# Kernel optimization log

Measured on AMD Instinct MI355X. Metric: run time of the kernel, lower is better.

Reference implementation:

```python
import jax, jax.numpy as jnp
import numpy as np

N_NODES = 50000
N_EDGES = 800000
IN_CH, HID_CH, OUT_CH = 128, 128, 64


def setup_inputs() -> dict:
    key = jax.random.key(0)
    k1, k2, k3, k4 = jax.random.split(key, 4)
    x = jax.random.normal(k1, (N_NODES, IN_CH), dtype=jnp.float32)
    edge_index = jax.random.randint(k2, (2, N_EDGES), 0, N_NODES, dtype=jnp.int64)
    W1 = jax.random.normal(k3, (IN_CH, HID_CH), dtype=jnp.float32) * (1.0 / np.sqrt(IN_CH))
    b1 = jnp.zeros((HID_CH,), dtype=jnp.float32)
    W2 = jax.random.normal(k4, (HID_CH, OUT_CH), dtype=jnp.float32) * (1.0 / np.sqrt(HID_CH))
    b2 = jnp.zeros((OUT_CH,), dtype=jnp.float32)
    return {"x": x, "edge_index": edge_index, "W1": W1, "b1": b1, "W2": W2, "b2": b2}


def _gcn_conv(x, src, dst, norm, W, b, n_nodes):
    # x' = D^-1/2 (A+I) D^-1/2 (x W) + b
    h = x @ W                                        # [N, C_out]
    msg = norm[:, None] * h[src]                     # gather + scale, [E', C_out]
    agg = jax.ops.segment_sum(msg, dst, num_segments=n_nodes)
    return agg + b


def reference(x, edge_index, W1, b1, W2, b2):
    n = x.shape[0]
    # add self loops
    loops = jnp.arange(n, dtype=edge_index.dtype)
    src = jnp.concatenate([edge_index[0], loops])
    dst = jnp.concatenate([edge_index[1], loops])
    # symmetric degree normalization computed on target index
    deg = jax.ops.segment_sum(jnp.ones_like(dst, dtype=x.dtype), dst, num_segments=n)
    dinv = jnp.where(deg > 0, jax.lax.rsqrt(deg), 0.0)
    norm = dinv[src] * dinv[dst]                     # [E']

    h = jax.nn.relu(_gcn_conv(x, src, dst, norm, W1, b1, n))
    logits = _gcn_conv(h, src, dst, norm, W2, b2, n)
    return jax.nn.softmax(logits, axis=1)
```

## Files before the change

### kernel.cpp

```cpp
#include <hip/hip_runtime.h>
#include <hip/hip_fp16.h>


#define SLOT 64
#define NB   49
#define CAP  18432
#define EPB  4096

typedef _Float16 h4 __attribute__((ext_vector_type(4)));
typedef _Float16 h8 __attribute__((ext_vector_type(8)));
typedef float f4 __attribute__((ext_vector_type(4)));

__global__ __launch_bounds__(256) void k_prep(const int* __restrict__ ei,
                                              int* __restrict__ bcur,
                                              unsigned int* __restrict__ bkt,
                                              const float* __restrict__ W1,
                                              const float* __restrict__ W2,
                                              _Float16* __restrict__ W1p,
                                              _Float16* __restrict__ W2p,
                                              int e, int pb) {
    __shared__ int sSrc[EPB];
    __shared__ int sDst[EPB];
    __shared__ int sCnt[64];
    if (blockIdx.x < pb) {
        int b0 = blockIdx.x * EPB;
        int cnt = min(EPB, e - b0);
        for (int i = threadIdx.x; i < cnt; i += 256) {
            sSrc[i] = ei[b0 + i];
            sDst[i] = ei[e + b0 + i];
        }
        if (threadIdx.x < 64) sCnt[threadIdx.x] = 0;
        __syncthreads();
        for (int i = threadIdx.x; i < cnt; i += 256)
            atomicAdd(&sCnt[sDst[i] >> 10], 1);
        __syncthreads();
        if (threadIdx.x < 64) {
            int c = sCnt[threadIdx.x];
            int gbase = (c > 0 && threadIdx.x < NB) ? atomicAdd(&bcur[threadIdx.x], c) : 0;
            sCnt[threadIdx.x] = gbase;
        }
        __syncthreads();
        for (int i = threadIdx.x; i < cnt; i += 256) {
            int d = sDst[i];
            int b = d >> 10;
            int pos = atomicAdd(&sCnt[b], 1);
            if (pos < CAP)
                bkt[(size_t)b * CAP + pos] =
                    ((unsigned int)(d & 1023) << 16) | (unsigned int)sSrc[i];
        }
    } else {
        int i = (blockIdx.x - pb) * 256 + threadIdx.x;
        float w; int k, c; _Float16* dst;
        if (i < 16384)      { k = i >> 7, c = i & 127; w = W1[i]; dst = W1p; }
        else if (i < 24576) { int t = i - 16384; k = t >> 6; c = t & 63; w = W2[t]; dst = W2p; }
        else return;
        _Float16 hi = (_Float16)w;
        _Float16 lo = (_Float16)(w - (float)hi);
        int kc = k >> 4, kk = k & 15;
        int l = (kk >> 2) * 16 + (c & 15);
        int j = kk & 3;
        int ct = c >> 4;
        size_t base = ((size_t)(ct * 8 + kc) * 64 + l) * 8 + j;
        dst[base] = hi;
        dst[base + 4] = lo;
    }
}

__global__ __launch_bounds__(256) void k_main1(
    const int* __restrict__ bcur, const unsigned int* __restrict__ bkt,
    unsigned short* __restrict__ csr, int* __restrict__ deg,
    float* __restrict__ dinv,
    const float* __restrict__ X, const _Float16* __restrict__ Wp,
    __half* __restrict__ H, int n, int bb)
{
    __shared__ unsigned short rows[256 * SLOT];
    __shared__ int cur[256];
    if (blockIdx.x < bb) {
        int r = blockIdx.x;
        int b = r >> 2;
        int q = r & 3;
        cur[threadIdx.x] = 0;
        __syncthreads();
        int cnt = min(bcur[b], CAP);
        const unsigned int* bp = bkt + (size_t)b * CAP;
        for (int i = threadIdx.x; i < cnt; i += 256) {
            unsigned int p = bp[i];
            int dl = (int)(p >> 16);
            if ((dl >> 8) == q) {
                int node = dl & 255;
                int pos = atomicAdd(&cur[node], 1);
                if (pos < SLOT) rows[node * SLOT + pos] = (unsigned short)(p & 0xffff);
            }
        }
        __syncthreads();
        int base = r * 256;
        uint4* dst4 = (uint4*)(csr + (size_t)base * SLOT);
        const uint4* src4 = (const uint4*)rows;
        for (int i = threadIdx.x; i < 256 * SLOT / 8; i += 256) dst4[i] = src4[i];
        int node = base + threadIdx.x;
        if (node < n) {
            int c = cur[threadIdx.x];
            deg[node] = c;
            dinv[node] = rsqrtf((float)(c + 1));
        }
    } else {
        int blk = blockIdx.x - bb;
        int w = threadIdx.x >> 6, lane = threadIdx.x & 63;
        int r0 = blk * 64 + w * 16;
        int xr = r0 + (lane & 15);
        int xrc = min(xr, n - 1);
        const float* xp = X + (size_t)xrc * 128 + ((lane >> 4) * 4);

        f4 acc[8];
#pragma unroll
        for (int ct = 0; ct < 8; ++ct) acc[ct] = (f4){0.f, 0.f, 0.f, 0.f};

#pragma unroll
        for (int kc = 0; kc < 8; ++kc) {
            float4 xv = *(const float4*)(xp + kc * 16);
            h4 xh, xl;
            xh[0] = (_Float16)xv.x; xh[1] = (_Float16)xv.y;
            xh[2] = (_Float16)xv.z; xh[3] = (_Float16)xv.w;
            xl[0] = (_Float16)(xv.x - (float)xh[0]);
            xl[1] = (_Float16)(xv.y - (float)xh[1]);
            xl[2] = (_Float16)(xv.z - (float)xh[2]);
            xl[3] = (_Float16)(xv.w - (float)xh[3]);
#pragma unroll
            for (int ct = 0; ct < 8; ++ct) {
                h8 wb = ((const h8*)Wp)[(ct * 8 + kc) * 64 + lane];
                h4 wh = {wb[0], wb[1], wb[2], wb[3]};
                h4 wl = {wb[4], wb[5], wb[6], wb[7]};
                acc[ct] = __builtin_amdgcn_mfma_f32_16x16x16f16(wh, xh, acc[ct], 0, 0, 0);
                acc[ct] = __builtin_amdgcn_mfma_f32_16x16x16f16(wl, xh, acc[ct], 0, 0, 0);
                acc[ct] = __builtin_amdgcn_mfma_f32_16x16x16f16(wh, xl, acc[ct], 0, 0, 0);
            }
        }
        if (xr < n) {
            __half* hp = H + (size_t)xr * 128 + (lane >> 4) * 4;
#pragma unroll
            for (int ct = 0; ct < 8; ++ct) {
                h4 o = {(_Float16)acc[ct][0], (_Float16)acc[ct][1],
                        (_Float16)acc[ct][2], (_Float16)acc[ct][3]};
                *(h4*)(hp + ct * 16) = o;
            }
        }
    }
}

__global__ __launch_bounds__(256) void k_agg1(
    const int* __restrict__ deg, const unsigned short* __restrict__ csr,
    const float* __restrict__ dinv, const __half* __restrict__ H,
    const float* __restrict__ b1, __half* __restrict__ H1, int n)
{
    int node = blockIdx.x * 4 + (threadIdx.x >> 6);
    if (node >= n) return;
    int lane = threadIdx.x & 63;
    int g = lane >> 4, sub = lane & 15;
    float dd = dinv[node];

    float acc[8];
#pragma unroll
    for (int i = 0; i < 8; ++i) acc[i] = 0.f;

    int beg = node * SLOT;
    int cnt = min(deg[node], SLOT);
    {
        int m = cnt;
        int   s_l = (lane < m) ? (int)csr[beg + lane] : 0;
        float w_l = (lane < m) ? dinv[s_l] * dd : 0.f;
        int iters = (m + 3) >> 2;
#pragma unroll 4
        for (int t = 0; t < iters; ++t) {
            int j = 4 * t + g;
            int   s = __shfl(s_l, j);
            float w = __shfl(w_l, j);
            float4 raw = ((const float4*)(H + (size_t)s * 128))[sub];
            const __half2* h2 = (const __half2*)&raw;
#pragma unroll
            for (int q = 0; q < 4; ++q) {
                float2 v = __half22float2(h2[q]);
                acc[2 * q]     = fmaf(w, v.x, acc[2 * q]);
                acc[2 * q + 1] = fmaf(w, v.y, acc[2 * q + 1]);
            }
        }
    }
#pragma unroll
    for (int i = 0; i < 8; ++i) {
        acc[i] += __shfl_xor(acc[i], 16);
        acc[i] += __shfl_xor(acc[i], 32);
    }
    float4 sraw = ((const float4*)(H + (size_t)node * 128))[sub];
    const __half2* sh2 = (const __half2*)&sraw;
    float sl = dd * dd;
    float4 bb0 = ((const float4*)(b1 + sub * 8))[0];
    float4 bb1 = ((const float4*)(b1 + sub * 8))[1];
    float out[8];
#pragma unroll
    for (int q = 0; q < 4; ++q) {
        float2 v = __half22float2(sh2[q]);
        out[2 * q]     = fmaf(sl, v.x, acc[2 * q]);
        out[2 * q + 1] = fmaf(sl, v.y, acc[2 * q + 1]);
    }
    out[0] += bb0.x; out[1] += bb0.y; out[2] += bb0.z; out[3] += bb0.w;
    out[4] += bb1.x; out[5] += bb1.y; out[6] += bb1.z; out[7] += bb1.w;
    if (g == 0) {
        h8 o;
#pragma unroll
        for (int i = 0; i < 8; ++i) o[i] = (_Float16)fmaxf(out[i], 0.f);
        *(h8*)(H1 + (size_t)node * 128 + sub * 8) = o;
    }
}

__global__ __launch_bounds__(256) void k_gemm2(
    const __half* __restrict__ Xh, const _Float16* __restrict__ Wp,
    __half* __restrict__ H2, int n)
{
    int w = threadIdx.x >> 6, lane = threadIdx.x & 63;
    int r0 = blockIdx.x * 64 + w * 16;
    int xr = r0 + (lane & 15);
    int xrc = min(xr, n - 1);
    const _Float16* xp = (const _Float16*)Xh + (size_t)xrc * 128 + ((lane >> 4) * 4);

    f4 acc[4];
#pragma unroll
    for (int ct = 0; ct < 4; ++ct) acc[ct] = (f4){0.f, 0.f, 0.f, 0.f};

#pragma unroll
    for (int kc = 0; kc < 8; ++kc) {
        h4 xh = *(const h4*)(xp + kc * 16);
#pragma unroll
        for (int ct = 0; ct < 4; ++ct) {
            h8 wb = ((const h8*)Wp)[(ct * 8 + kc) * 64 + lane];
            h4 wh = {wb[0], wb[1], wb[2], wb[3]};
            h4 wl = {wb[4], wb[5], wb[6], wb[7]};
            acc[ct] = __builtin_amdgcn_mfma_f32_16x16x16f16(wh, xh, acc[ct], 0, 0, 0);
            acc[ct] = __builtin_amdgcn_mfma_f32_16x16x16f16(wl, xh, acc[ct], 0, 0, 0);
        }
    }
    if (xr < n) {
        __half* hp = H2 + (size_t)xr * 64 + (lane >> 4) * 4;
#pragma unroll
        for (int ct = 0; ct < 4; ++ct) {
            h4 o = {(_Float16)acc[ct][0], (_Float16)acc[ct][1],
                    (_Float16)acc[ct][2], (_Float16)acc[ct][3]};
            *(h4*)(hp + ct * 16) = o;
        }
    }
}

__global__ __launch_bounds__(256) void k_agg2(
    const int* __restrict__ deg, const unsigned short* __restrict__ csr,
    const float* __restrict__ dinv, const __half* __restrict__ H2,
    const float* __restrict__ b2, float* __restrict__ OUT, int n)
{
    int node = blockIdx.x * 4 + (threadIdx.x >> 6);
    if (node >= n) return;
    int lane = threadIdx.x & 63;
    int g = lane >> 3, sub = lane & 7;
    float dd = dinv[node];

    float acc[8];
#pragma unroll
    for (int i = 0; i < 8; ++i) acc[i] = 0.f;

    int beg = node * SLOT;
    int cnt = min(deg[node], SLOT);
    {
        int m = cnt;
        int   s_l = (lane < m) ? (int)csr[beg + lane] : 0;
        float w_l = (lane < m) ? dinv[s_l] * dd : 0.f;
        int iters = (m + 7) >> 3;
#pragma unroll 4
        for (int t = 0; t < iters; ++t) {
            int j = 8 * t + g;
            int   s = __shfl(s_l, j);
            float w = __shfl(w_l, j);
            float4 raw = ((const float4*)(H2 + (size_t)s * 64))[sub];
            const __half2* h2 = (const __half2*)&raw;
#pragma unroll
            for (int q = 0; q < 4; ++q) {
                float2 v = __half22float2(h2[q]);
                acc[2 * q]     = fmaf(w, v.x, acc[2 * q]);
                acc[2 * q + 1] = fmaf(w, v.y, acc[2 * q + 1]);
            }
        }
    }
#pragma unroll
    for (int i = 0; i < 8; ++i) {
        acc[i] += __shfl_xor(acc[i], 8);
        acc[i] += __shfl_xor(acc[i], 16);
        acc[i] += __shfl_xor(acc[i], 32);
    }
    float4 sraw = ((const float4*)(H2 + (size_t)node * 64))[sub];
    const __half2* sh2 = (const __half2*)&sraw;
    float sl = dd * dd;
    float4 bb0 = ((const float4*)(b2 + sub * 8))[0];
    float4 bb1 = ((const float4*)(b2 + sub * 8))[1];
    float out[8];
#pragma unroll
    for (int q = 0; q < 4; ++q) {
        float2 v = __half22float2(sh2[q]);
        out[2 * q]     = fmaf(sl, v.x, acc[2 * q]);
        out[2 * q + 1] = fmaf(sl, v.y, acc[2 * q + 1]);
    }
    out[0] += bb0.x; out[1] += bb0.y; out[2] += bb0.z; out[3] += bb0.w;
    out[4] += bb1.x; out[5] += bb1.y; out[6] += bb1.z; out[7] += bb1.w;
    float mx = out[0];
#pragma unroll
    for (int i = 1; i < 8; ++i) mx = fmaxf(mx, out[i]);
    mx = fmaxf(mx, __shfl_xor(mx, 1));
    mx = fmaxf(mx, __shfl_xor(mx, 2));
    mx = fmaxf(mx, __shfl_xor(mx, 4));
    float sm = 0.f;
#pragma unroll
    for (int i = 0; i < 8; ++i) { out[i] = expf(out[i] - mx); sm += out[i]; }
    sm += __shfl_xor(sm, 1);
    sm += __shfl_xor(sm, 2);
    sm += __shfl_xor(sm, 4);
    float inv = 1.f / sm;
#pragma unroll
    for (int i = 0; i < 8; ++i) out[i] *= inv;
    float* op = OUT + (size_t)node * 64 + sub * 8;
    if (g == 0) *(float4*)op       = make_float4(out[0], out[1], out[2], out[3]);
    if (g == 1) *(float4*)(op + 4) = make_float4(out[4], out[5], out[6], out[7]);
}

extern "C" void kernel_launch(void* const* d_in, const int* in_sizes, int n_in,
                              void* d_out, int out_size, void* d_ws, size_t ws_size,
                              hipStream_t stream) {
    const float* X  = (const float*)d_in[0];
    const int*   EI = (const int*)d_in[1];
    const float* W1 = (const float*)d_in[2];
    const float* B1 = (const float*)d_in[3];
    const float* W2 = (const float*)d_in[4];
    const float* B2 = (const float*)d_in[5];
    float* OUT = (float*)d_out;

    const int n = in_sizes[0] / 128;
    const int e = in_sizes[1] / 2;

    const int np = (n + 255) & ~255;
    int*            bcur = (int*)d_ws;
    int*            deg  = bcur + 64;
    float*          dinv = (float*)(deg + np);
    unsigned int*   bkt  = (unsigned int*)(dinv + np);
    unsigned short* csr  = (unsigned short*)(bkt + (size_t)NB * CAP);
    _Float16*       W1p  = (_Float16*)(csr + (size_t)np * SLOT);
    _Float16*       W2p  = W1p + 32768;
    __half*         H16  = (__half*)(W2p + 16384);
    __half*         H1   = (__half*)(H16 + (size_t)np * 128);
    __half*         H2   = H1 + (size_t)np * 128;

    const int pb = (e + EPB - 1) / EPB;
    const int bb = np / 256;
    const int gb = (n + 63) / 64;

    (void)hipMemsetAsync(bcur, 0, 64 * sizeof(int), stream);
    k_prep<<<pb + 96, 256, 0, stream>>>(EI, bcur, bkt, W1, W2, W1p, W2p, e, pb);
    k_main1<<<bb + gb, 256, 0, stream>>>(bcur, bkt, csr, deg, dinv,
                                         X, W1p, H16, n, bb);
    k_agg1<<<(n + 3) / 4, 256, 0, stream>>>(deg, csr, dinv, H16, B1, H1, n);
    k_gemm2<<<gb, 256, 0, stream>>>(H1, W2p, H2, n);
    k_agg2<<<(n + 3) / 4, 256, 0, stream>>>(deg, csr, dinv, H2, B2, OUT, n);
}
```

Measured before the change: 194.1 us.

## Fuse second-layer GEMM into first aggregation kernel using wave shuffles

Replaces the separate MFMA GEMM for layer 2 with per-node shuffle-broadcast FMAs inside the layer-1 aggregation kernel, writing H2 directly. This removes the H1 intermediate's global write and reread and one kernel launch, and drops W2 prepacking. In exchange, every wave does 128 shuffles and 128 W2 loads per node on scalar FMA units instead of tensor cores, which may make the aggregation kernel compute- or load-bound.

```diff
diff --git a/kernel.cpp b/kernel.cpp
--- a/kernel.cpp
+++ b/kernel.cpp
@@ -15,14 +15,12 @@
                                               int* __restrict__ bcur,
                                               unsigned int* __restrict__ bkt,
                                               const float* __restrict__ W1,
-                                              const float* __restrict__ W2,
                                               _Float16* __restrict__ W1p,
-                                              _Float16* __restrict__ W2p,
                                               int e, int pb) {
     __shared__ int sSrc[EPB];
     __shared__ int sDst[EPB];
     __shared__ int sCnt[64];
-    if (blockIdx.x < pb) {
+    if ((int)blockIdx.x < pb) {
         int b0 = blockIdx.x * EPB;
         int cnt = min(EPB, e - b0);
         for (int i = threadIdx.x; i < cnt; i += 256) {
@@ -50,10 +48,9 @@
         }
     } else {
         int i = (blockIdx.x - pb) * 256 + threadIdx.x;
-        float w; int k, c; _Float16* dst;
-        if (i < 16384)      { k = i >> 7, c = i & 127; w = W1[i]; dst = W1p; }
-        else if (i < 24576) { int t = i - 16384; k = t >> 6; c = t & 63; w = W2[t]; dst = W2p; }
-        else return;
+        if (i >= 16384) return;
+        int k = i >> 7, c = i & 127;
+        float w = W1[i];
         _Float16 hi = (_Float16)w;
         _Float16 lo = (_Float16)(w - (float)hi);
         int kc = k >> 4, kk = k & 15;
@@ -61,8 +58,8 @@
         int j = kk & 3;
         int ct = c >> 4;
         size_t base = ((size_t)(ct * 8 + kc) * 64 + l) * 8 + j;
-        dst[base] = hi;
-        dst[base + 4] = lo;
+        W1p[base] = hi;
+        W1p[base + 4] = lo;
     }
 }
 
@@ -75,7 +72,7 @@
 {
     __shared__ unsigned short rows[256 * SLOT];
     __shared__ int cur[256];
-    if (blockIdx.x < bb) {
+    if ((int)blockIdx.x < bb) {
         int r = blockIdx.x;
         int b = r >> 2;
         int q = r & 3;
@@ -114,7 +111,6 @@
         f4 acc[8];
 #pragma unroll
         for (int ct = 0; ct < 8; ++ct) acc[ct] = (f4){0.f, 0.f, 0.f, 0.f};
-
 #pragma unroll
         for (int kc = 0; kc < 8; ++kc) {
             float4 xv = *(const float4*)(xp + kc * 16);
@@ -147,10 +143,11 @@
     }
 }
 
-__global__ __launch_bounds__(256) void k_agg1(
+__global__ __launch_bounds__(256) void k_agg1g2(
     const int* __restrict__ deg, const unsigned short* __restrict__ csr,
     const float* __restrict__ dinv, const __half* __restrict__ H,
-    const float* __restrict__ b1, __half* __restrict__ H1, int n)
+    const float* __restrict__ b1, const float* __restrict__ W2,
+    __half* __restrict__ H2, int n)
 {
     int node = blockIdx.x * 4 + (threadIdx.x >> 6);
     if (node >= n) return;
@@ -203,49 +200,19 @@
     }
     out[0] += bb0.x; out[1] += bb0.y; out[2] += bb0.z; out[3] += bb0.w;
     out[4] += bb1.x; out[5] += bb1.y; out[6] += bb1.z; out[7] += bb1.w;
-    if (g == 0) {
-        h8 o;
-#pragma unroll
-        for (int i = 0; i < 8; ++i) o[i] = (_Float16)fmaxf(out[i], 0.f);
-        *(h8*)(H1 + (size_t)node * 128 + sub * 8) = o;
-    }
-}
-
-__global__ __launch_bounds__(256) void k_gemm2(
-    const __half* __restrict__ Xh, const _Float16* __restrict__ Wp,
-    __half* __restrict__ H2, int n)
-{
-    int w = threadIdx.x >> 6, lane = threadIdx.x & 63;
-    int r0 = blockIdx.x * 64 + w * 16;
-    int xr = r0 + (lane & 15);
-    int xrc = min(xr, n - 1);
-    const _Float16* xp = (const _Float16*)Xh + (size_t)xrc * 128 + ((lane >> 4) * 4);
-
-    f4 acc[4];
-#pragma unroll
-    for (int ct = 0; ct < 4; ++ct) acc[ct] = (f4){0.f, 0.f, 0.f, 0.f};
-
-#pragma unroll
-    for (int kc = 0; kc < 8; ++kc) {
-        h4 xh = *(const h4*)(xp + kc * 16);
-#pragma unroll
-        for (int ct = 0; ct < 4; ++ct) {
-            h8 wb = ((const h8*)Wp)[(ct * 8 + kc) * 64 + lane];
-            h4 wh = {wb[0], wb[1], wb[2], wb[3]};
-            h4 wl = {wb[4], wb[5], wb[6], wb[7]};
-            acc[ct] = __builtin_amdgcn_mfma_f32_16x16x16f16(wh, xh, acc[ct], 0, 0, 0);
-            acc[ct] = __builtin_amdgcn_mfma_f32_16x16x16f16(wl, xh, acc[ct], 0, 0, 0);
-        }
-    }
-    if (xr < n) {
-        __half* hp = H2 + (size_t)xr * 64 + (lane >> 4) * 4;
-#pragma unroll
-        for (int ct = 0; ct < 4; ++ct) {
-            h4 o = {(_Float16)acc[ct][0], (_Float16)acc[ct][1],
-                    (_Float16)acc[ct][2], (_Float16)acc[ct][3]};
-            *(h4*)(hp + ct * 16) = o;
-        }
-    }
+#pragma unroll
+    for (int i = 0; i < 8; ++i) out[i] = fmaxf(out[i], 0.f);
+
+    float o2 = 0.f;
+#pragma unroll
+    for (int i = 0; i < 8; ++i) {
+#pragma unroll
+        for (int s = 0; s < 16; ++s) {
+            float h1k = __shfl(out[i], s);
+            o2 = fmaf(h1k, W2[(s * 8 + i) * 64 + lane], o2);
+        }
+    }
+    H2[(size_t)node * 64 + lane] = (__half)o2;
 }
 
 __global__ __launch_bounds__(256) void k_agg2(
@@ -346,20 +313,17 @@
     unsigned int*   bkt  = (unsigned int*)(dinv + np);
     unsigned short* csr  = (unsigned short*)(bkt + (size_t)NB * CAP);
     _Float16*       W1p  = (_Float16*)(csr + (size_t)np * SLOT);
-    _Float16*       W2p  = W1p + 32768;
-    __half*         H16  = (__half*)(W2p + 16384);
-    __half*         H1   = (__half*)(H16 + (size_t)np * 128);
-    __half*         H2   = H1 + (size_t)np * 128;
+    __half*         H16  = (__half*)(W1p + 32768);
+    __half*         H2   = H16 + (size_t)np * 128;
 
     const int pb = (e + EPB - 1) / EPB;
     const int bb = np / 256;
     const int gb = (n + 63) / 64;
 
     (void)hipMemsetAsync(bcur, 0, 64 * sizeof(int), stream);
-    k_prep<<<pb + 96, 256, 0, stream>>>(EI, bcur, bkt, W1, W2, W1p, W2p, e, pb);
+    k_prep<<<pb + 64, 256, 0, stream>>>(EI, bcur, bkt, W1, W1p, e, pb);
     k_main1<<<bb + gb, 256, 0, stream>>>(bcur, bkt, csr, deg, dinv,
                                          X, W1p, H16, n, bb);
-    k_agg1<<<(n + 3) / 4, 256, 0, stream>>>(deg, csr, dinv, H16, B1, H1, n);
-    k_gemm2<<<gb, 256, 0, stream>>>(H1, W2p, H2, n);
+    k_agg1g2<<<(n + 3) / 4, 256, 0, stream>>>(deg, csr, dinv, H16, B1, W2, H2, n);
     k_agg2<<<(n + 3) / 4, 256, 0, stream>>>(deg, csr, dinv, H2, B2, OUT, n);
 }
```

After: 251.9 us. 1.3x slower.
